# Optimization experiments

Measured on AMD Instinct MI355X. Metric: run time of the kernel, lower is better.

## Reference

```python
import jax, jax.numpy as jnp
import numpy as np

HID = 512

def setup_inputs() -> dict:
    key = jax.random.key(0)
    k1, k2, k3, k4, k5, k6 = jax.random.split(key, 6)
    B, T, H = 32, 4096, HID
    enc_seq = jax.random.normal(k1, (B, T, H), dtype=jnp.float32)
    enc_mask = jax.random.randint(k2, (B, T), 0, 2, dtype=jnp.int32)
    dec_state = jax.random.normal(k3, (B, H), dtype=jnp.float32)
    # Linear weights, torch layout: y = x @ W.T
    scale = 1.0 / np.sqrt(H)
    W_h = jax.random.uniform(k4, (H, H), jnp.float32, -scale, scale)
    W_s = jax.random.uniform(k5, (H, H), jnp.float32, -scale, scale)
    v = jax.random.uniform(k6, (H,), jnp.float32, -scale, scale)
    return {"enc_seq": enc_seq, "enc_mask": enc_mask, "dec_state": dec_state,
            "W_h": W_h, "W_s": W_s, "v": v}

def reference(enc_seq, enc_mask, dec_state, W_h, W_s, v):
    # s: [B,H] -> [B,1,H] broadcast over T; h: [B,T,H]
    s = jnp.einsum('bh,kh->bk', dec_state, W_s)[:, None, :]
    h = jnp.einsum('bth,kh->btk', enc_seq, W_h)
    e = jnp.einsum('bth,h->bt', jnp.tanh(h + s), v)  # [B,T]
    e = jnp.where(enc_mask == 0, jnp.float32(-1e9), e)
    a = jax.nn.softmax(e, axis=1)  # [B,T]
    ctx = jnp.einsum('bt,bth->bh', a, enc_seq)  # [B,H]
    return (ctx, a)
```

## Files before the change

kernel.cpp:

```cpp
#include <hip/hip_runtime.h>
#include <hip/hip_bf16.h>
#include <cstdint>
#include <cstddef>

#define HID 512
#define T_SZ 4096

typedef __bf16 bf16x8 __attribute__((ext_vector_type(8)));
typedef float f32x4 __attribute__((ext_vector_type(4)));

__device__ __forceinline__ unsigned short f2bf_rne(float f) {
    unsigned int u = __float_as_uint(f);
    unsigned int r = (u + 0x7FFFu + ((u >> 16) & 1u)) >> 16;
    return (unsigned short)r;
}

__device__ __forceinline__ bf16x8 pack8(float4 x0, float4 x1) {
    bf16x8 r;
    r[0] = (__bf16)x0.x; r[1] = (__bf16)x0.y; r[2] = (__bf16)x0.z; r[3] = (__bf16)x0.w;
    r[4] = (__bf16)x1.x; r[5] = (__bf16)x1.y; r[6] = (__bf16)x1.z; r[7] = (__bf16)x1.w;
    return r;
}

__device__ __forceinline__ float fast_tanh(float x) {
    float e = __expf(2.0f * x);
    return 1.0f - 2.0f / (e + 1.0f);
}

__global__ void k_s(const float* __restrict__ dec, const float* __restrict__ Ws,
                    float* __restrict__ s) {
    int idx = blockIdx.x * 256 + threadIdx.x;
    int b = idx >> 9, n = idx & 511;
    const float4* dp = reinterpret_cast<const float4*>(dec + (size_t)b * HID);
    const float4* wp = reinterpret_cast<const float4*>(Ws + (size_t)n * HID);
    float acc = 0.f;
#pragma unroll 8
    for (int i = 0; i < HID / 4; ++i) {
        float4 d = dp[i], w = wp[i];
        acc += d.x * w.x + d.y * w.y + d.z * w.z + d.w * w.w;
    }
    s[idx] = acc;
}

__global__ void k_pack(const float* __restrict__ Wh, uint4* __restrict__ Wb) {
    int idx = blockIdx.x * 256 + threadIdx.x;
    int n = idx >> 6;
    int k0 = (idx & 63) * 8;
    const float4* p = reinterpret_cast<const float4*>(Wh + (size_t)n * HID + k0);
    float4 x0 = p[0], x1 = p[1];
    uint4 w;
    w.x = f2bf_rne(x0.x) | ((unsigned)f2bf_rne(x0.y) << 16);
    w.y = f2bf_rne(x0.z) | ((unsigned)f2bf_rne(x0.w) << 16);
    w.z = f2bf_rne(x1.x) | ((unsigned)f2bf_rne(x1.y) << 16);
    w.w = f2bf_rne(x1.z) | ((unsigned)f2bf_rne(x1.w) << 16);
    int n4 = n >> 4, c = n & 15, kk = k0 >> 5, g = (k0 >> 3) & 3;
    Wb[(size_t)kk * 2048 + n4 * 64 + g * 16 + c] = w;
}

__global__ void __launch_bounds__(512, 4) k_gemm_e(
    const float* __restrict__ enc, const uint4* __restrict__ Wb,
    const float* __restrict__ s, const float* __restrict__ v,
    float* __restrict__ part_e) {
    __shared__ __align__(16) unsigned char As[65536];
    __shared__ float red[2][4][32];

    const int tid = threadIdx.x;
    const int p = blockIdx.x;
    const int logical = (p & 7) * 512 + (p >> 3);
    const int h = logical & 1;
    const int m = logical >> 1;
    const size_t row0 = (size_t)m * 64;
    const int b = (int)(row0 >> 12);

    const int lane = tid & 63, wid = tid >> 6;
    const int c = lane & 15, g4 = lane >> 4;
    const int wm = wid >> 2, wn = wid & 3;

    float sv_s[4], sv_v[4];
#pragma unroll
    for (int ni = 0; ni < 4; ++ni) {
        int n = (h * 16 + wn * 4 + ni) * 16 + c;
        sv_s[ni] = s[b * HID + n];
        sv_v[ni] = v[n];
    }

    {
        const float* base = enc + row0 * HID;
#pragma unroll
        for (int i = 0; i < 8; ++i) {
            int G = i * 512 + tid;
            int kk = G >> 8, cin = G & 255;
            int mi = cin >> 6, gg = (cin >> 4) & 3, cc = cin & 15;
            const float* src = base + (size_t)(mi * 16 + cc) * HID + kk * 32 + gg * 8;
            float4 x0 = *reinterpret_cast<const float4*>(src);
            float4 x1 = *reinterpret_cast<const float4*>(src + 4);
            *reinterpret_cast<bf16x8*>(&As[G * 16]) = pack8(x0, x1);
        }
    }
    __syncthreads();

    const uint4* Bg = Wb + (size_t)(h * 16 + wn * 4) * 64 + lane;

    uint4 bR[2][4];
#pragma unroll
    for (int d = 0; d < 2; ++d)
#pragma unroll
        for (int ni = 0; ni < 4; ++ni)
            bR[d][ni] = Bg[(size_t)d * 2048 + ni * 64];

    bf16x8 af[2][2];
#pragma unroll
    for (int mi = 0; mi < 2; ++mi)
        af[0][mi] = *reinterpret_cast<const bf16x8*>(&As[((wm * 2 + mi) * 64 + lane) * 16]);

    f32x4 acc[2][4] = {};

#pragma unroll
    for (int kk = 0; kk < 16; ++kk) {
        if (kk < 15) {
#pragma unroll
            for (int mi = 0; mi < 2; ++mi)
                af[(kk + 1) & 1][mi] = *reinterpret_cast<const bf16x8*>(
                    &As[(kk + 1) * 4096 + ((wm * 2 + mi) * 64 + lane) * 16]);
        }
#pragma unroll
        for (int mi = 0; mi < 2; ++mi)
#pragma unroll
            for (int ni = 0; ni < 4; ++ni)
                acc[mi][ni] = __builtin_amdgcn_mfma_f32_16x16x32_bf16(
                    af[kk & 1][mi], *reinterpret_cast<bf16x8*>(&bR[kk & 1][ni]),
                    acc[mi][ni], 0, 0, 0);
        if (kk + 2 <= 15) {
#pragma unroll
            for (int ni = 0; ni < 4; ++ni)
                bR[kk & 1][ni] = Bg[(size_t)(kk + 2) * 2048 + ni * 64];
        }
    }

    float e_part[2][4] = {};
#pragma unroll
    for (int ni = 0; ni < 4; ++ni) {
        float sn = sv_s[ni], vn = sv_v[ni];
#pragma unroll
        for (int mi = 0; mi < 2; ++mi)
#pragma unroll
            for (int r = 0; r < 4; ++r)
                e_part[mi][r] += fast_tanh(acc[mi][ni][r] + sn) * vn;
    }
#pragma unroll
    for (int mm = 1; mm <= 8; mm <<= 1)
#pragma unroll
        for (int mi = 0; mi < 2; ++mi)
#pragma unroll
            for (int r = 0; r < 4; ++r)
                e_part[mi][r] += __shfl_xor(e_part[mi][r], mm);

    if (c == 0) {
#pragma unroll
        for (int mi = 0; mi < 2; ++mi)
#pragma unroll
            for (int r = 0; r < 4; ++r)
                red[wm][wn][mi * 16 + g4 * 4 + r] = e_part[mi][r];
    }
    __syncthreads();
    if (tid < 64) {
        int wm2 = tid >> 5, rl = tid & 31;
        part_e[(size_t)h * 131072 + row0 + tid] =
            red[wm2][0][rl] + red[wm2][1][rl] + red[wm2][2][rl] + red[wm2][3][rl];
    }
}

__global__ void k_softmax(const float* __restrict__ part_e, float* __restrict__ a,
                          const int* __restrict__ mask) {
    int b = blockIdx.x, tid = threadIdx.x;
    int lane = tid & 63, wid = tid >> 6;
    __shared__ float red[16];
    float vals[4]; int ms[4];
    float mx = -1e30f;
#pragma unroll
    for (int j = 0; j < 4; ++j) {
        size_t t = (size_t)b * T_SZ + tid + j * 1024;
        vals[j] = part_e[t] + part_e[131072 + t];
        ms[j] = mask[t];
        if (ms[j]) mx = fmaxf(mx, vals[j]);
    }
#pragma unroll
    for (int m = 32; m >= 1; m >>= 1) mx = fmaxf(mx, __shfl_xor(mx, m));
    if (lane == 0) red[wid] = mx;
    __syncthreads();
    if (tid == 0) {
        float m2 = red[0];
        for (int i = 1; i < 16; ++i) m2 = fmaxf(m2, red[i]);
        red[0] = m2;
    }
    __syncthreads();
    mx = red[0];
    __syncthreads();
    float pv[4]; float sum = 0.f;
#pragma unroll
    for (int j = 0; j < 4; ++j) { pv[j] = ms[j] ? __expf(vals[j] - mx) : 0.f; sum += pv[j]; }
#pragma unroll
    for (int m = 32; m >= 1; m >>= 1) sum += __shfl_xor(sum, m);
    if (lane == 0) red[wid] = sum;
    __syncthreads();
    if (tid == 0) {
        float s2 = 0.f;
        for (int i = 0; i < 16; ++i) s2 += red[i];
        red[0] = s2;
    }
    __syncthreads();
    float inv = 1.f / red[0];
#pragma unroll
    for (int j = 0; j < 4; ++j)
        a[(size_t)b * T_SZ + tid + j * 1024] = pv[j] * inv;
}

__global__ void k_ctx(const float* __restrict__ enc, const float* __restrict__ a,
                      float2* __restrict__ part) {
    int ts = blockIdx.x, b = blockIdx.y, tid = threadIdx.x;
    size_t rbase = (size_t)b * T_SZ + (size_t)ts * 128;
    const float2* ep = reinterpret_cast<const float2*>(enc + rbase * HID) + tid;
    const float* ap = a + rbase;
    float ax = 0.f, ay = 0.f, bx = 0.f, by = 0.f;
#pragma unroll 2
    for (int t = 0; t < 128; t += 2) {
        float a0 = ap[t], a1 = ap[t + 1];
        float2 e0 = ep[(size_t)t * 256], e1 = ep[(size_t)(t + 1) * 256];
        ax += a0 * e0.x; ay += a0 * e0.y;
        bx += a1 * e1.x; by += a1 * e1.y;
    }
    float2 r; r.x = ax + bx; r.y = ay + by;
    part[(size_t)(b * 32 + ts) * 256 + tid] = r;
}

__global__ void k_ctxred(const float* __restrict__ part, float* __restrict__ ctx) {
    int idx = blockIdx.x * 256 + threadIdx.x;
    int b = idx >> 9, h = idx & 511;
    float sum = 0.f;
#pragma unroll
    for (int ts = 0; ts < 32; ++ts) sum += part[(size_t)(b * 32 + ts) * 512 + h];
    ctx[idx] = sum;
}

extern "C" void kernel_launch(void* const* d_in, const int* in_sizes, int n_in,
                              void* d_out, int out_size, void* d_ws, size_t ws_size,
                              hipStream_t stream) {
    const float* enc  = (const float*)d_in[0];
    const int*   mask = (const int*)d_in[1];
    const float* dec  = (const float*)d_in[2];
    const float* Wh   = (const float*)d_in[3];
    const float* Ws   = (const float*)d_in[4];
    const float* v    = (const float*)d_in[5];

    float* out = (float*)d_out;
    float* ctx = out;
    float* a   = out + 16384;

    float* ws     = (float*)d_ws;
    float* s      = ws;
    uint4* Wb     = (uint4*)(ws + 16384);
    float* part_e = ws + 16384 + 131072;
    float* part   = part_e + 262144;

    hipLaunchKernelGGL(k_s,      dim3(64),      dim3(256),  0, stream, dec, Ws, s);
    hipLaunchKernelGGL(k_pack,   dim3(128),     dim3(256),  0, stream, Wh, Wb);
    hipLaunchKernelGGL(k_gemm_e, dim3(4096),    dim3(512),  0, stream, enc, Wb, s, v, part_e);
    hipLaunchKernelGGL(k_softmax,dim3(32),      dim3(1024), 0, stream, part_e, a, mask);
    hipLaunchKernelGGL(k_ctx,    dim3(32, 32),  dim3(256),  0, stream, enc, a, (float2*)part);
    hipLaunchKernelGGL(k_ctxred, dim3(64),      dim3(256),  0, stream, part, ctx);
}
```

Measured before the change: 214.1 us.

## Enlarge GEMM M-tile to 256 rows with double-buffered K pipeline

The fused tanh-attention GEMM now gives each block a 256x256 output tile instead of 64x256. The K dimension is streamed in 64-wide stages, with A and B double-buffered in LDS. B is loaded straight into LDS with global_load_lds, A is prefetched into registers and converted while MFMAs run, and s_setprio raises priority around the MFMA groups. The aim is to reuse each B tile across more rows and to overlap global loads with compute. In exchange, accumulator registers grow, occupancy drops to 2 blocks per CU, and the grid shrinks to 1024 blocks.

```diff
diff --git a/kernel.cpp b/kernel.cpp
--- a/kernel.cpp
+++ b/kernel.cpp
@@ -25,6 +25,12 @@
 __device__ __forceinline__ float fast_tanh(float x) {
     float e = __expf(2.0f * x);
     return 1.0f - 2.0f / (e + 1.0f);
+}
+
+__device__ __forceinline__ void gload_lds16(const void* g, void* l) {
+    __builtin_amdgcn_global_load_lds(
+        (const __attribute__((address_space(1))) unsigned int*)g,
+        (__attribute__((address_space(3))) unsigned int*)l, 16, 0, 0);
 }
 
 __global__ void k_s(const float* __restrict__ dec, const float* __restrict__ Ws,
@@ -57,92 +63,122 @@
     Wb[(size_t)kk * 2048 + n4 * 64 + g * 16 + c] = w;
 }
 
-__global__ void __launch_bounds__(512, 4) k_gemm_e(
+__global__ void __launch_bounds__(512, 2) k_gemm_e(
     const float* __restrict__ enc, const uint4* __restrict__ Wb,
     const float* __restrict__ s, const float* __restrict__ v,
     float* __restrict__ part_e) {
-    __shared__ __align__(16) unsigned char As[65536];
-    __shared__ float red[2][4][32];
+    __shared__ __align__(16) unsigned char Abuf[2][32768];
+    __shared__ __align__(16) unsigned char Bbuf[2][32768];
+    __shared__ float red[4][256];
 
     const int tid = threadIdx.x;
     const int p = blockIdx.x;
-    const int logical = (p & 7) * 512 + (p >> 3);
+    const int logical = (p & 7) * 128 + (p >> 3);
     const int h = logical & 1;
-    const int m = logical >> 1;
-    const size_t row0 = (size_t)m * 64;
+    const int mt = logical >> 1;
+    const size_t row0 = (size_t)mt * 256;
     const int b = (int)(row0 >> 12);
 
     const int lane = tid & 63, wid = tid >> 6;
-    const int c = lane & 15, g4 = lane >> 4;
+    const int c16 = lane & 15, g4 = lane >> 4;
     const int wm = wid >> 2, wn = wid & 3;
 
     float sv_s[4], sv_v[4];
 #pragma unroll
     for (int ni = 0; ni < 4; ++ni) {
-        int n = (h * 16 + wn * 4 + ni) * 16 + c;
+        int n = h * 256 + wn * 64 + ni * 16 + c16;
         sv_s[ni] = s[b * HID + n];
         sv_v[ni] = v[n];
     }
 
-    {
-        const float* base = enc + row0 * HID;
-#pragma unroll
-        for (int i = 0; i < 8; ++i) {
-            int G = i * 512 + tid;
-            int kk = G >> 8, cin = G & 255;
-            int mi = cin >> 6, gg = (cin >> 4) & 3, cc = cin & 15;
-            const float* src = base + (size_t)(mi * 16 + cc) * HID + kk * 32 + gg * 8;
-            float4 x0 = *reinterpret_cast<const float4*>(src);
-            float4 x1 = *reinterpret_cast<const float4*>(src + 4);
-            *reinterpret_cast<bf16x8*>(&As[G * 16]) = pack8(x0, x1);
+    const float* Asrc[4];
+    int Adst[4];
+#pragma unroll
+    for (int i = 0; i < 4; ++i) {
+        int ch = tid + i * 512;
+        int kk2 = ch >> 10, rem = ch & 1023;
+        int rt = rem >> 6, g = (rem >> 4) & 3, cc = rem & 15;
+        Asrc[i] = enc + (row0 + rt * 16 + cc) * HID + kk2 * 32 + g * 8;
+        Adst[i] = ch * 16;
+    }
+
+    float4 ar[8];
+
+#pragma unroll
+    for (int r = 0; r < 4; ++r) {
+        int j = wid * 4 + r, kk2 = j >> 4, n4o = j & 15;
+        gload_lds16(Wb + (size_t)kk2 * 2048 + (h * 16 + n4o) * 64 + lane,
+                    &Bbuf[0][(kk2 * 1024 + n4o * 64) * 16]);
+    }
+#pragma unroll
+    for (int i = 0; i < 4; ++i) {
+        ar[2 * i]     = *reinterpret_cast<const float4*>(Asrc[i]);
+        ar[2 * i + 1] = *reinterpret_cast<const float4*>(Asrc[i] + 4);
+    }
+#pragma unroll
+    for (int i = 0; i < 4; ++i)
+        *reinterpret_cast<bf16x8*>(&Abuf[0][Adst[i]]) = pack8(ar[2 * i], ar[2 * i + 1]);
+    asm volatile("s_waitcnt lgkmcnt(0)\n\ts_barrier" ::: "memory");
+
+    f32x4 acc[8][4] = {};
+
+#pragma unroll
+    for (int t = 0; t < 8; ++t) {
+        const int cur = t & 1, nxt = cur ^ 1;
+        if (t < 7) {
+#pragma unroll
+            for (int r = 0; r < 4; ++r) {
+                int j = wid * 4 + r, kk2 = j >> 4, n4o = j & 15;
+                gload_lds16(Wb + (size_t)(2 * (t + 1) + kk2) * 2048
+                                + (h * 16 + n4o) * 64 + lane,
+                            &Bbuf[nxt][(kk2 * 1024 + n4o * 64) * 16]);
+            }
+#pragma unroll
+            for (int i = 0; i < 4; ++i) {
+                ar[2 * i]     = *reinterpret_cast<const float4*>(Asrc[i] + (t + 1) * 64);
+                ar[2 * i + 1] = *reinterpret_cast<const float4*>(Asrc[i] + (t + 1) * 64 + 4);
+            }
         }
-    }
-    __syncthreads();
-
-    const uint4* Bg = Wb + (size_t)(h * 16 + wn * 4) * 64 + lane;
-
-    uint4 bR[2][4];
-#pragma unroll
-    for (int d = 0; d < 2; ++d)
-#pragma unroll
-        for (int ni = 0; ni < 4; ++ni)
-            bR[d][ni] = Bg[(size_t)d * 2048 + ni * 64];
-
-    bf16x8 af[2][2];
-#pragma unroll
-    for (int mi = 0; mi < 2; ++mi)
-        af[0][mi] = *reinterpret_cast<const bf16x8*>(&As[((wm * 2 + mi) * 64 + lane) * 16]);
-
-    f32x4 acc[2][4] = {};
-
-#pragma unroll
-    for (int kk = 0; kk < 16; ++kk) {
-        if (kk < 15) {
-#pragma unroll
-            for (int mi = 0; mi < 2; ++mi)
-                af[(kk + 1) & 1][mi] = *reinterpret_cast<const bf16x8*>(
-                    &As[(kk + 1) * 4096 + ((wm * 2 + mi) * 64 + lane) * 16]);
+#pragma unroll
+        for (int kk2 = 0; kk2 < 2; ++kk2) {
+            bf16x8 bfr[4];
+#pragma unroll
+            for (int ni = 0; ni < 4; ++ni)
+                bfr[ni] = *reinterpret_cast<const bf16x8*>(
+                    &Bbuf[cur][(kk2 * 1024 + (wn * 4 + ni) * 64 + lane) * 16]);
+#pragma unroll
+            for (int mh = 0; mh < 2; ++mh) {
+                bf16x8 afr[4];
+#pragma unroll
+                for (int i = 0; i < 4; ++i)
+                    afr[i] = *reinterpret_cast<const bf16x8*>(
+                        &Abuf[cur][(kk2 * 1024 + (wm * 8 + mh * 4 + i) * 64 + lane) * 16]);
+                __builtin_amdgcn_s_setprio(1);
+#pragma unroll
+                for (int i = 0; i < 4; ++i)
+#pragma unroll
+                    for (int ni = 0; ni < 4; ++ni)
+                        acc[mh * 4 + i][ni] = __builtin_amdgcn_mfma_f32_16x16x32_bf16(
+                            afr[i], bfr[ni], acc[mh * 4 + i][ni], 0, 0, 0);
+                __builtin_amdgcn_s_setprio(0);
+            }
         }
-#pragma unroll
-        for (int mi = 0; mi < 2; ++mi)
-#pragma unroll
-            for (int ni = 0; ni < 4; ++ni)
-                acc[mi][ni] = __builtin_amdgcn_mfma_f32_16x16x32_bf16(
-                    af[kk & 1][mi], *reinterpret_cast<bf16x8*>(&bR[kk & 1][ni]),
-                    acc[mi][ni], 0, 0, 0);
-        if (kk + 2 <= 15) {
-#pragma unroll
-            for (int ni = 0; ni < 4; ++ni)
-                bR[kk & 1][ni] = Bg[(size_t)(kk + 2) * 2048 + ni * 64];
+        if (t < 7) {
+            __builtin_amdgcn_sched_barrier(0);
+#pragma unroll
+            for (int i = 0; i < 4; ++i)
+                *reinterpret_cast<bf16x8*>(&Abuf[nxt][Adst[i]]) =
+                    pack8(ar[2 * i], ar[2 * i + 1]);
+            asm volatile("s_waitcnt lgkmcnt(0)\n\ts_barrier" ::: "memory");
         }
     }
 
-    float e_part[2][4] = {};
+    float e_part[8][4] = {};
 #pragma unroll
     for (int ni = 0; ni < 4; ++ni) {
         float sn = sv_s[ni], vn = sv_v[ni];
 #pragma unroll
-        for (int mi = 0; mi < 2; ++mi)
+        for (int mi = 0; mi < 8; ++mi)
 #pragma unroll
             for (int r = 0; r < 4; ++r)
                 e_part[mi][r] += fast_tanh(acc[mi][ni][r] + sn) * vn;
@@ -150,24 +186,22 @@
 #pragma unroll
     for (int mm = 1; mm <= 8; mm <<= 1)
 #pragma unroll
-        for (int mi = 0; mi < 2; ++mi)
+        for (int mi = 0; mi < 8; ++mi)
 #pragma unroll
             for (int r = 0; r < 4; ++r)
                 e_part[mi][r] += __shfl_xor(e_part[mi][r], mm);
 
-    if (c == 0) {
-#pragma unroll
-        for (int mi = 0; mi < 2; ++mi)
+    if (c16 == 0) {
+#pragma unroll
+        for (int mi = 0; mi < 8; ++mi)
 #pragma unroll
             for (int r = 0; r < 4; ++r)
-                red[wm][wn][mi * 16 + g4 * 4 + r] = e_part[mi][r];
-    }
-    __syncthreads();
-    if (tid < 64) {
-        int wm2 = tid >> 5, rl = tid & 31;
+                red[wn][wm * 128 + mi * 16 + g4 * 4 + r] = e_part[mi][r];
+    }
+    __syncthreads();
+    if (tid < 256)
         part_e[(size_t)h * 131072 + row0 + tid] =
-            red[wm2][0][rl] + red[wm2][1][rl] + red[wm2][2][rl] + red[wm2][3][rl];
-    }
+            red[0][tid] + red[1][tid] + red[2][tid] + red[3][tid];
 }
 
 __global__ void k_softmax(const float* __restrict__ part_e, float* __restrict__ a,
@@ -264,7 +298,7 @@
 
     hipLaunchKernelGGL(k_s,      dim3(64),      dim3(256),  0, stream, dec, Ws, s);
     hipLaunchKernelGGL(k_pack,   dim3(128),     dim3(256),  0, stream, Wh, Wb);
-    hipLaunchKernelGGL(k_gemm_e, dim3(4096),    dim3(512),  0, stream, enc, Wb, s, v, part_e);
+    hipLaunchKernelGGL(k_gemm_e, dim3(1024),    dim3(512),  0, stream, enc, Wb, s, v, part_e);
     hipLaunchKernelGGL(k_softmax,dim3(32),      dim3(1024), 0, stream, part_e, a, mask);
     hipLaunchKernelGGL(k_ctx,    dim3(32, 32),  dim3(256),  0, stream, enc, a, (float2*)part);
     hipLaunchKernelGGL(k_ctxred, dim3(64),      dim3(256),  0, stream, part, ctx);
```

Result: no change. 217.7 us (+1.6%).
